# Performance work log

Hardware: AMD Instinct MI355X
Metric: run time of the kernel (lower is better)

Reference implementation:

```python
import jax, jax.numpy as jnp
import numpy as np

NUM_NODES = 100000
EMBED_DIM = 128
HIDDEN = 128
NUM_EDGES = 1600000


def gcn_conv(x, W, b, src, dst, num_nodes):
    """PyG GCNConv: x' = D^{-1/2} (A+I) D^{-1/2} (x W) + b, symmetric norm with self-loops."""
    x = x @ W  # [N, out]
    loops = jnp.arange(num_nodes, dtype=src.dtype)
    s = jnp.concatenate([src, loops])  # sources incl. self-loops
    d = jnp.concatenate([dst, loops])  # targets incl. self-loops
    deg = jax.ops.segment_sum(jnp.ones_like(d, dtype=x.dtype), d, num_segments=num_nodes)
    dis = jnp.where(deg > 0, jax.lax.rsqrt(deg), 0.0)  # deg^{-1/2}, 0 where isolated
    norm = dis[s] * dis[d]  # [E+N]
    msg = x[s] * norm[:, None]  # gather + scale
    out = jax.ops.segment_sum(msg, d, num_segments=num_nodes)  # scatter-add
    return out + b


def setup_inputs() -> dict:
    key = jax.random.key(0)
    k1, k2, k3, k4, k5, k6 = jax.random.split(key, 6)
    edge_index = jax.random.randint(k1, (2, NUM_EDGES), 0, NUM_NODES, dtype=jnp.int64)
    edge_attr = jax.random.normal(k2, (NUM_EDGES,), dtype=jnp.float32)
    emb = jax.random.normal(k3, (NUM_NODES, EMBED_DIM), dtype=jnp.float32) * 0.1
    W1 = jax.random.normal(k4, (EMBED_DIM, HIDDEN), dtype=jnp.float32) * (1.0 / np.sqrt(EMBED_DIM))
    b1 = jnp.zeros((HIDDEN,), dtype=jnp.float32)
    W2 = jax.random.normal(k5, (HIDDEN, HIDDEN), dtype=jnp.float32) * (1.0 / np.sqrt(HIDDEN))
    b2 = jnp.zeros((HIDDEN,), dtype=jnp.float32)
    return {"edge_index": edge_index, "edge_attr": edge_attr, "emb": emb,
            "W1": W1, "b1": b1, "W2": W2, "b2": b2}


def reference(edge_index, edge_attr, emb, W1, b1, W2, b2):
    src, dst = edge_index[0], edge_index[1]
    x = gcn_conv(emb, W1, b1, src, dst, NUM_NODES)
    x = jax.nn.relu(x)
    x = gcn_conv(x, W2, b2, src, dst, NUM_NODES)
    return x
```

## Files before the change

kernel.cpp:

```cpp
#include <hip/hip_runtime.h>

#define EMB 128
#define NBUC 1024
#define NPART 256
#define NSEG 8
#define SEGLEN (NPART / NSEG)
#define PREPB 128

typedef __attribute__((ext_vector_type(8))) short short8;
typedef __attribute__((ext_vector_type(4))) float f32x4;

__device__ __forceinline__ unsigned short f2bf(float f) {
    union { float f; unsigned int i; } v; v.f = f;
    unsigned int x = v.i;
    x += 0x7fffu + ((x >> 16) & 1u);
    return (unsigned short)(x >> 16);
}
__device__ __forceinline__ void acc_fma4(uint2 v, float d,
                                         float& a0, float& a1, float& a2, float& a3) {
    union { unsigned int i; float f; } t;
    t.i = v.x << 16;          a0 = fmaf(d, t.f, a0);
    t.i = v.x & 0xffff0000u;  a1 = fmaf(d, t.f, a1);
    t.i = v.y << 16;          a2 = fmaf(d, t.f, a2);
    t.i = v.y & 0xffff0000u;  a3 = fmaf(d, t.f, a3);
}


__device__ __forceinline__ void p1_body(int bid, int* h, const int* __restrict__ dst,
                                        int* __restrict__ BH, int E, int chunk) {
    for (int i = threadIdx.x; i < NBUC; i += 256) h[i] = 0;
    __syncthreads();
    int s = bid * chunk;
    int e = min(E, s + chunk);
    for (int i = s + threadIdx.x; i < e; i += 256)
        atomicAdd(&h[dst[i] >> 7], 1);
    __syncthreads();
    for (int i = threadIdx.x; i < NBUC; i += 256)
        BH[bid * NBUC + i] = h[i];
}

__device__ __forceinline__ void prepw_body(int bid, const float* __restrict__ W1,
                                           const float* __restrict__ W2,
                                           unsigned short* __restrict__ W1s,
                                           unsigned short* __restrict__ W2s) {
    int gid = bid * 256 + threadIdx.x;
    const float* W = (gid < 16384) ? W1 : W2;
    unsigned short* Ws = (gid < 16384) ? W1s : W2s;
    int idx = gid & 16383;
    int k = idx >> 7, n = idx & 127;
    int kk = k >> 5, q = (k >> 3) & 3, j = k & 7;
    int ct = n >> 4, nn = n & 15;
    int didx = ((((kk * 8 + ct) * 4 + q) * 16 + nn) << 3) + j;
    Ws[didx] = f2bf(W[idx]);
}

__global__ __launch_bounds__(256) void k_start(const int* __restrict__ dst,
                                               int* __restrict__ BH, int E, int chunk,
                                               const float* __restrict__ W1,
                                               const float* __restrict__ W2,
                                               unsigned short* __restrict__ W1s,
                                               unsigned short* __restrict__ W2s) {
    __shared__ int h[NBUC];
    int b = blockIdx.x;
    if (b < NPART) p1_body(b, h, dst, BH, E, chunk);
    else           prepw_body(b - NPART, W1, W2, W1s, W2s);
}

__global__ __launch_bounds__(256) void p_segsum(const int* __restrict__ BH,
                                                int* __restrict__ SS) {
    int idx = blockIdx.x * 256 + threadIdx.x;
    int seg = idx >> 10, b = idx & (NBUC - 1);
    int s = 0;
#pragma unroll 8
    for (int k = 0; k < SEGLEN; ++k)
        s += BH[(seg * SEGLEN + k) * NBUC + b];
    SS[seg * NBUC + b] = s;
}

__global__ __launch_bounds__(1024) void p_scan(const int* __restrict__ SS,
                                               int* __restrict__ base, int E) {
    __shared__ int a[NBUC];
    int t = threadIdx.x;
    int v0 = 0;
#pragma unroll 8
    for (int s = 0; s < NSEG; ++s) v0 += SS[s * NBUC + t];
    a[t] = v0;
    __syncthreads();
    for (int off = 1; off < NBUC; off <<= 1) {
        int v = (t >= off) ? a[t - off] : 0;
        __syncthreads();
        a[t] += v;
        __syncthreads();
    }
    base[t] = a[t] - v0;
    if (t == NBUC - 1) base[NBUC] = E;
}

__global__ __launch_bounds__(256) void p_offs2(int* __restrict__ BH,
                                               const int* __restrict__ SS,
                                               const int* __restrict__ base) {
    int idx = blockIdx.x * 256 + threadIdx.x;
    int seg = idx >> 10, b = idx & (NBUC - 1);
    int run = base[b];
    for (int s = 0; s < seg; ++s) run += SS[s * NBUC + b];
#pragma unroll 4
    for (int k = 0; k < SEGLEN; ++k) {
        int* p = &BH[(seg * SEGLEN + k) * NBUC + b];
        int v = *p;
        *p = run;
        run += v;
    }
}

__device__ __forceinline__ void scatter_body(int bid, int* cnt,
                                             const int* __restrict__ src,
                                             const int* __restrict__ dst,
                                             const int* __restrict__ BH,
                                             int* __restrict__ part,
                                             int E, int chunk) {
    for (int i = threadIdx.x; i < NBUC; i += 256)
        cnt[i] = BH[bid * NBUC + i];
    __syncthreads();
    int s = bid * chunk;
    int e = min(E, s + chunk);
    for (int i = s + threadIdx.x; i < e; i += 256) {
        int d = dst[i];
        int pos = atomicAdd(&cnt[d >> 7], 1);
        part[pos] = src[i] | ((d & 127) << 17);
    }
}

__global__ __launch_bounds__(256) void p3_csr(const int* __restrict__ part,
                                              const int* __restrict__ base,
                                              int* __restrict__ R, int* __restrict__ adj,
                                              float* __restrict__ dis, int N, int E) {
    __shared__ int hist[128];
    __shared__ int sc[128];
    __shared__ int cnt[128];
    int b = blockIdx.x;
    int n0 = b * 128;
    int nn = min(128, N - n0);
    int s = base[b], e = base[b + 1];
    int t = threadIdx.x;

    if (t < 128) hist[t] = 0;
    __syncthreads();
    for (int i = s + t; i < e; i += 256)
        atomicAdd(&hist[part[i] >> 17], 1);
    __syncthreads();

    if (t < 128) sc[t] = hist[t];
    __syncthreads();
    for (int off = 1; off < 128; off <<= 1) {
        int v = 0;
        if (t < 128 && t >= off) v = sc[t - off];
        __syncthreads();
        if (t < 128) sc[t] += v;
        __syncthreads();
    }
    if (t < 128) {
        int excl = sc[t] - hist[t];
        cnt[t] = excl;
        if (t < nn) {
            R[n0 + t] = s + excl;
            dis[n0 + t] = rsqrtf((float)hist[t] + 1.0f);
        }
    }
    if (b == 0 && t == 0) R[N] = E;
    __syncthreads();

    for (int i = s + t; i < e; i += 256) {
        int p = part[i];
        int pos = atomicAdd(&cnt[p >> 17], 1);
        adj[s + pos] = p & 0x1FFFF;
    }
}

template <bool XBF16>
__device__ __forceinline__ void gemm_body(int bid, unsigned short* lds,
    const void* Xv, const unsigned short* __restrict__ Wsw,
    unsigned short* __restrict__ Y, int N)
{
    {
        const uint4* srcp = (const uint4*)Wsw;
        uint4* dstp = (uint4*)lds;
        for (int i = threadIdx.x; i < 2048; i += 256) dstp[i] = srcp[i];
    }
    __syncthreads();

    const int wave = threadIdx.x >> 6;
    const int lane = threadIdx.x & 63;
    const int q = lane >> 4, nn = lane & 15;
    const int row0 = bid * 64 + wave * 16;
    const int arow = row0 + nn;
    const int arc = arow < N ? arow : N - 1;

    f32x4 acc[8];
#pragma unroll
    for (int ct = 0; ct < 8; ++ct) acc[ct] = (f32x4){0.f, 0.f, 0.f, 0.f};

#pragma unroll
    for (int kk = 0; kk < 4; ++kk) {
        short8 af;
        if (XBF16) {
            af = *(const short8*)((const unsigned short*)Xv + (size_t)arc * EMB + kk * 32 + q * 8);
        } else {
            const float* xp = (const float*)Xv + (size_t)arc * EMB + kk * 32 + q * 8;
            float4 u0 = *(const float4*)xp;
            float4 u1 = *(const float4*)(xp + 4);
            af[0] = (short)f2bf(u0.x); af[1] = (short)f2bf(u0.y);
            af[2] = (short)f2bf(u0.z); af[3] = (short)f2bf(u0.w);
            af[4] = (short)f2bf(u1.x); af[5] = (short)f2bf(u1.y);
            af[6] = (short)f2bf(u1.z); af[7] = (short)f2bf(u1.w);
        }
#pragma unroll
        for (int ct = 0; ct < 8; ++ct) {
            short8 bf = ((const short8*)lds)[(kk * 8 + ct) * 64 + lane];
            acc[ct] = __builtin_amdgcn_mfma_f32_16x16x32_bf16(af, bf, acc[ct], 0, 0, 0);
        }
    }

    __syncthreads();

#pragma unroll
    for (int ct = 0; ct < 8; ++ct) {
#pragma unroll
        for (int r = 0; r < 4; ++r) {
            int ml = wave * 16 + q * 4 + r;
            lds[ml * 136 + ct * 16 + nn] = f2bf(acc[ct][r]);
        }
    }
    __syncthreads();

    const int rbase = bid * 64;
    for (int i = threadIdx.x; i < 1024; i += 256) {
        int row = i >> 4, off = i & 15;
        int grow = rbase + row;
        if (grow < N) {
            uint4 v = *(const uint4*)(lds + row * 136 + off * 8);
            *((uint4*)(Y + (size_t)grow * EMB) + off) = v;
        }
    }
}

__global__ __launch_bounds__(256) void k_mid(
    const int* __restrict__ src, const int* __restrict__ dstp,
    const int* __restrict__ BH, int* __restrict__ part, int E, int chunk,
    const void* Xv, const unsigned short* __restrict__ W1s,
    unsigned short* __restrict__ Y, int N)
{
    __shared__ __align__(16) unsigned short smem[16384];
    int b = blockIdx.x;
    if (b < NPART) scatter_body(b, (int*)smem, src, dstp, BH, part, E, chunk);
    else           gemm_body<false>(b - NPART, smem, Xv, W1s, Y, N);
}

__global__ __launch_bounds__(256) void k_gemm2(
    const void* Xv, const unsigned short* __restrict__ Wsw,
    unsigned short* __restrict__ Y, int N)
{
    __shared__ __align__(16) unsigned short smem[16384];
    gemm_body<true>(blockIdx.x, smem, Xv, Wsw, Y, N);
}

template <bool RELU, bool BF16OUT>
__global__ __launch_bounds__(256) void k_gather_finalize(
    const int* __restrict__ R, const int* __restrict__ adj,
    const unsigned short* __restrict__ Y, const float* __restrict__ dis,
    const float* __restrict__ bias, void* __restrict__ Outv, int N)
{
    int t = blockIdx.x * 256 + threadIdx.x;
    int n = t >> 5;
    if (n >= N) return;
    int j = (t & 31) * 4;

    int rs = R[n], re = R[n + 1];
    float dv = dis[n];

    float a0 = 0.f, a1 = 0.f, a2 = 0.f, a3 = 0.f;
    uint2 sv = *(const uint2*)(Y + (size_t)n * EMB + j);
    acc_fma4(sv, dv, a0, a1, a2, a3);

    int e = rs;
    for (; e + 3 < re; e += 4) {
        int s0 = adj[e], s1 = adj[e + 1], s2 = adj[e + 2], s3 = adj[e + 3];
        float d0 = dis[s0], d1 = dis[s1], d2 = dis[s2], d3 = dis[s3];
        uint2 v0 = *(const uint2*)(Y + (size_t)s0 * EMB + j);
        uint2 v1 = *(const uint2*)(Y + (size_t)s1 * EMB + j);
        uint2 v2 = *(const uint2*)(Y + (size_t)s2 * EMB + j);
        uint2 v3 = *(const uint2*)(Y + (size_t)s3 * EMB + j);
        acc_fma4(v0, d0, a0, a1, a2, a3);
        acc_fma4(v1, d1, a0, a1, a2, a3);
        acc_fma4(v2, d2, a0, a1, a2, a3);
        acc_fma4(v3, d3, a0, a1, a2, a3);
    }
    for (; e < re; ++e) {
        int s0 = adj[e];
        float d0 = dis[s0];
        uint2 v0 = *(const uint2*)(Y + (size_t)s0 * EMB + j);
        acc_fma4(v0, d0, a0, a1, a2, a3);
    }

    float4 b = *(const float4*)(bias + j);
    float o0 = dv * a0 + b.x;
    float o1 = dv * a1 + b.y;
    float o2 = dv * a2 + b.z;
    float o3 = dv * a3 + b.w;
    if (RELU) {
        o0 = fmaxf(o0, 0.f); o1 = fmaxf(o1, 0.f);
        o2 = fmaxf(o2, 0.f); o3 = fmaxf(o3, 0.f);
    }
    if (BF16OUT) {
        ushort4 o = { f2bf(o0), f2bf(o1), f2bf(o2), f2bf(o3) };
        *(ushort4*)((unsigned short*)Outv + (size_t)n * EMB + j) = o;
    } else {
        float4 o = { o0, o1, o2, o3 };
        *(float4*)((float*)Outv + (size_t)n * EMB + j) = o;
    }
}

extern "C" void kernel_launch(void* const* d_in, const int* in_sizes, int n_in,
                              void* d_out, int out_size, void* d_ws, size_t ws_size,
                              hipStream_t stream) {
    const int* ei = (const int*)d_in[0];
    const int E = in_sizes[0] / 2;
    const float* emb = (const float*)d_in[2];
    const int N = in_sizes[2] / EMB;
    const float* W1 = (const float*)d_in[3];
    const float* b1 = (const float*)d_in[4];
    const float* W2 = (const float*)d_in[5];
    const float* b2 = (const float*)d_in[6];
    float* out = (float*)d_out;

    const int* src = ei;
    const int* dstp = ei + E;

    char* w = (char*)d_ws;
    auto take = [&](size_t bytes) { char* p = w; w += (bytes + 511) & ~(size_t)511; return p; };
    float* dis  = (float*)take((size_t)N * 4);
    int*   R    = (int*)  take((size_t)(N + 1) * 4);
    int*   base = (int*)  take((size_t)(NBUC + 1) * 4);
    int*   SS   = (int*)  take((size_t)NSEG * NBUC * 4);
    int*   adj  = (int*)  take((size_t)E * 4);
    unsigned short* W1s = (unsigned short*)take((size_t)EMB * EMB * 2);
    unsigned short* W2s = (unsigned short*)take((size_t)EMB * EMB * 2);
    unsigned short* Hb  = (unsigned short*)take((size_t)N * EMB * 2);
    int*   part = (int*)Hb;
    int*   BH   = (int*)((char*)Hb + (((size_t)E * 4 + 511) & ~(size_t)511));
    unsigned short* Y1b = (unsigned short*)d_out;

    const int NB = (N + 127) / 128;
    const int chunk = (E + NPART - 1) / NPART;
    const int gM = (N + 63) / 64;
    const int gG = (N * 32 + 255) / 256;
    const int gS = (NSEG * NBUC) / 256;

    k_start   <<<NPART + PREPB, 256, 0, stream>>>(dstp, BH, E, chunk, W1, W2, W1s, W2s);
    p_segsum  <<<gS, 256, 0, stream>>>(BH, SS);
    p_scan    <<<1, NBUC, 0, stream>>>(SS, base, E);
    p_offs2   <<<gS, 256, 0, stream>>>(BH, SS, base);

    k_mid     <<<NPART + gM, 256, 0, stream>>>(src, dstp, BH, part, E, chunk,
                                               emb, W1s, Y1b, N);
    p3_csr    <<<NB, 256, 0, stream>>>(part, base, R, adj, dis, N, E);

    k_gather_finalize<true, true><<<gG, 256, 0, stream>>>(R, adj, Y1b, dis, b1, Hb, N);

    k_gemm2<<<gM, 256, 0, stream>>>(Hb, W2s, Hb, N);
    k_gather_finalize<false, false><<<gG, 256, 0, stream>>>(R, adj, Hb, dis, b2, out, N);
}
```

Measured before the change: 327.7 us.

## Replace per-partition offset scan with global atomics; fold layer-2 source norm into GEMM

The bucket-offset pipeline changes from per-partition histograms plus segment-sum and offset kernels to a global atomic histogram, a single scan, and per-block atomic reservation of bucket ranges during scatter. This removes two kernel launches and the BH buffer traffic, but the scatter pass now reads dst twice. The layer-2 GEMM now multiplies each output row by dis[row], so the second gather can sum plain bf16 rows without looking up dis per neighbour. The gather loops are also unrolled to 8 neighbours to keep more loads in flight. Edge order inside buckets becomes nondeterministic, but the CSR build re-sorts within each bucket.

```diff
diff --git a/kernel.cpp b/kernel.cpp
--- a/kernel.cpp
+++ b/kernel.cpp
@@ -3,8 +3,6 @@
 #define EMB 128
 #define NBUC 1024
 #define NPART 256
-#define NSEG 8
-#define SEGLEN (NPART / NSEG)
 #define PREPB 128
 
 typedef __attribute__((ext_vector_type(8))) short short8;
@@ -24,10 +22,18 @@
     t.i = v.y << 16;          a2 = fmaf(d, t.f, a2);
     t.i = v.y & 0xffff0000u;  a3 = fmaf(d, t.f, a3);
 }
+__device__ __forceinline__ void acc_bf4(uint2 v,
+                                        float& a0, float& a1, float& a2, float& a3) {
+    union { unsigned int i; float f; } t;
+    t.i = v.x << 16;          a0 += t.f;
+    t.i = v.x & 0xffff0000u;  a1 += t.f;
+    t.i = v.y << 16;          a2 += t.f;
+    t.i = v.y & 0xffff0000u;  a3 += t.f;
+}
 
 
 __device__ __forceinline__ void p1_body(int bid, int* h, const int* __restrict__ dst,
-                                        int* __restrict__ BH, int E, int chunk) {
+                                        int* __restrict__ tot, int E, int chunk) {
     for (int i = threadIdx.x; i < NBUC; i += 256) h[i] = 0;
     __syncthreads();
     int s = bid * chunk;
@@ -35,8 +41,10 @@
     for (int i = s + threadIdx.x; i < e; i += 256)
         atomicAdd(&h[dst[i] >> 7], 1);
     __syncthreads();
-    for (int i = threadIdx.x; i < NBUC; i += 256)
-        BH[bid * NBUC + i] = h[i];
+    for (int i = threadIdx.x; i < NBUC; i += 256) {
+        int v = h[i];
+        if (v) atomicAdd(&tot[i], v);
+    }
 }
 
 __device__ __forceinline__ void prepw_body(int bid, const float* __restrict__ W1,
@@ -55,35 +63,23 @@
 }
 
 __global__ __launch_bounds__(256) void k_start(const int* __restrict__ dst,
-                                               int* __restrict__ BH, int E, int chunk,
+                                               int* __restrict__ tot, int E, int chunk,
                                                const float* __restrict__ W1,
                                                const float* __restrict__ W2,
                                                unsigned short* __restrict__ W1s,
                                                unsigned short* __restrict__ W2s) {
     __shared__ int h[NBUC];
     int b = blockIdx.x;
-    if (b < NPART) p1_body(b, h, dst, BH, E, chunk);
+    if (b < NPART) p1_body(b, h, dst, tot, E, chunk);
     else           prepw_body(b - NPART, W1, W2, W1s, W2s);
 }
 
-__global__ __launch_bounds__(256) void p_segsum(const int* __restrict__ BH,
-                                                int* __restrict__ SS) {
-    int idx = blockIdx.x * 256 + threadIdx.x;
-    int seg = idx >> 10, b = idx & (NBUC - 1);
-    int s = 0;
-#pragma unroll 8
-    for (int k = 0; k < SEGLEN; ++k)
-        s += BH[(seg * SEGLEN + k) * NBUC + b];
-    SS[seg * NBUC + b] = s;
-}
-
-__global__ __launch_bounds__(1024) void p_scan(const int* __restrict__ SS,
-                                               int* __restrict__ base, int E) {
+__global__ __launch_bounds__(1024) void p_scan(const int* __restrict__ tot,
+                                               int* __restrict__ base,
+                                               int* __restrict__ gcnt, int E) {
     __shared__ int a[NBUC];
     int t = threadIdx.x;
-    int v0 = 0;
-#pragma unroll 8
-    for (int s = 0; s < NSEG; ++s) v0 += SS[s * NBUC + t];
+    int v0 = tot[t];
     a[t] = v0;
     __syncthreads();
     for (int off = 1; off < NBUC; off <<= 1) {
@@ -92,37 +88,30 @@
         a[t] += v;
         __syncthreads();
     }
-    base[t] = a[t] - v0;
+    int excl = a[t] - v0;
+    base[t] = excl;
+    gcnt[t] = excl;
     if (t == NBUC - 1) base[NBUC] = E;
-}
-
-__global__ __launch_bounds__(256) void p_offs2(int* __restrict__ BH,
-                                               const int* __restrict__ SS,
-                                               const int* __restrict__ base) {
-    int idx = blockIdx.x * 256 + threadIdx.x;
-    int seg = idx >> 10, b = idx & (NBUC - 1);
-    int run = base[b];
-    for (int s = 0; s < seg; ++s) run += SS[s * NBUC + b];
-#pragma unroll 4
-    for (int k = 0; k < SEGLEN; ++k) {
-        int* p = &BH[(seg * SEGLEN + k) * NBUC + b];
-        int v = *p;
-        *p = run;
-        run += v;
-    }
 }
 
 __device__ __forceinline__ void scatter_body(int bid, int* cnt,
                                              const int* __restrict__ src,
                                              const int* __restrict__ dst,
-                                             const int* __restrict__ BH,
+                                             int* __restrict__ gcnt,
                                              int* __restrict__ part,
                                              int E, int chunk) {
-    for (int i = threadIdx.x; i < NBUC; i += 256)
-        cnt[i] = BH[bid * NBUC + i];
+    for (int i = threadIdx.x; i < NBUC; i += 256) cnt[i] = 0;
     __syncthreads();
     int s = bid * chunk;
     int e = min(E, s + chunk);
+    for (int i = s + threadIdx.x; i < e; i += 256)
+        atomicAdd(&cnt[dst[i] >> 7], 1);
+    __syncthreads();
+    for (int i = threadIdx.x; i < NBUC; i += 256) {
+        int c = cnt[i];
+        cnt[i] = c ? atomicAdd(&gcnt[i], c) : 0;
+    }
+    __syncthreads();
     for (int i = s + threadIdx.x; i < e; i += 256) {
         int d = dst[i];
         int pos = atomicAdd(&cnt[d >> 7], 1);
@@ -176,10 +165,10 @@
     }
 }
 
-template <bool XBF16>
+template <bool XBF16, bool SCALE>
 __device__ __forceinline__ void gemm_body(int bid, unsigned short* lds,
     const void* Xv, const unsigned short* __restrict__ Wsw,
-    unsigned short* __restrict__ Y, int N)
+    const float* __restrict__ dis, unsigned short* __restrict__ Y, int N)
 {
     {
         const uint4* srcp = (const uint4*)Wsw;
@@ -222,12 +211,21 @@
 
     __syncthreads();
 
+    float dv[4];
+    if (SCALE) {
+#pragma unroll
+        for (int r = 0; r < 4; ++r) {
+            int gm = row0 + q * 4 + r;
+            dv[r] = dis[gm < N ? gm : N - 1];
+        }
+    }
 #pragma unroll
     for (int ct = 0; ct < 8; ++ct) {
 #pragma unroll
         for (int r = 0; r < 4; ++r) {
             int ml = wave * 16 + q * 4 + r;
-            lds[ml * 136 + ct * 16 + nn] = f2bf(acc[ct][r]);
+            float val = SCALE ? acc[ct][r] * dv[r] : acc[ct][r];
+            lds[ml * 136 + ct * 16 + nn] = f2bf(val);
         }
     }
     __syncthreads();
@@ -245,25 +243,25 @@
 
 __global__ __launch_bounds__(256) void k_mid(
     const int* __restrict__ src, const int* __restrict__ dstp,
-    const int* __restrict__ BH, int* __restrict__ part, int E, int chunk,
+    int* __restrict__ gcnt, int* __restrict__ part, int E, int chunk,
     const void* Xv, const unsigned short* __restrict__ W1s,
     unsigned short* __restrict__ Y, int N)
 {
     __shared__ __align__(16) unsigned short smem[16384];
     int b = blockIdx.x;
-    if (b < NPART) scatter_body(b, (int*)smem, src, dstp, BH, part, E, chunk);
-    else           gemm_body<false>(b - NPART, smem, Xv, W1s, Y, N);
+    if (b < NPART) scatter_body(b, (int*)smem, src, dstp, gcnt, part, E, chunk);
+    else           gemm_body<false, false>(b - NPART, smem, Xv, W1s, nullptr, Y, N);
 }
 
 __global__ __launch_bounds__(256) void k_gemm2(
     const void* Xv, const unsigned short* __restrict__ Wsw,
-    unsigned short* __restrict__ Y, int N)
+    const float* __restrict__ dis, unsigned short* __restrict__ Y, int N)
 {
     __shared__ __align__(16) unsigned short smem[16384];
-    gemm_body<true>(blockIdx.x, smem, Xv, Wsw, Y, N);
-}
-
-template <bool RELU, bool BF16OUT>
+    gemm_body<true, true>(blockIdx.x, smem, Xv, Wsw, dis, Y, N);
+}
+
+template <bool FOLD, bool RELU, bool BF16OUT>
 __global__ __launch_bounds__(256) void k_gather_finalize(
     const int* __restrict__ R, const int* __restrict__ adj,
     const unsigned short* __restrict__ Y, const float* __restrict__ dis,
@@ -279,26 +277,55 @@
 
     float a0 = 0.f, a1 = 0.f, a2 = 0.f, a3 = 0.f;
     uint2 sv = *(const uint2*)(Y + (size_t)n * EMB + j);
-    acc_fma4(sv, dv, a0, a1, a2, a3);
+    if (FOLD) acc_fma4(sv, dv, a0, a1, a2, a3);
+    else      acc_bf4(sv, a0, a1, a2, a3);
 
     int e = rs;
-    for (; e + 3 < re; e += 4) {
-        int s0 = adj[e], s1 = adj[e + 1], s2 = adj[e + 2], s3 = adj[e + 3];
-        float d0 = dis[s0], d1 = dis[s1], d2 = dis[s2], d3 = dis[s3];
+    for (; e + 7 < re; e += 8) {
+        int s0 = adj[e],     s1 = adj[e + 1], s2 = adj[e + 2], s3 = adj[e + 3];
+        int s4 = adj[e + 4], s5 = adj[e + 5], s6 = adj[e + 6], s7 = adj[e + 7];
         uint2 v0 = *(const uint2*)(Y + (size_t)s0 * EMB + j);
         uint2 v1 = *(const uint2*)(Y + (size_t)s1 * EMB + j);
         uint2 v2 = *(const uint2*)(Y + (size_t)s2 * EMB + j);
         uint2 v3 = *(const uint2*)(Y + (size_t)s3 * EMB + j);
-        acc_fma4(v0, d0, a0, a1, a2, a3);
-        acc_fma4(v1, d1, a0, a1, a2, a3);
-        acc_fma4(v2, d2, a0, a1, a2, a3);
-        acc_fma4(v3, d3, a0, a1, a2, a3);
+        uint2 v4 = *(const uint2*)(Y + (size_t)s4 * EMB + j);
+        uint2 v5 = *(const uint2*)(Y + (size_t)s5 * EMB + j);
+        uint2 v6 = *(const uint2*)(Y + (size_t)s6 * EMB + j);
+        uint2 v7 = *(const uint2*)(Y + (size_t)s7 * EMB + j);
+        if (FOLD) {
+            float d0 = dis[s0], d1 = dis[s1], d2 = dis[s2], d3 = dis[s3];
+            float d4 = dis[s4], d5 = dis[s5], d6 = dis[s6], d7 = dis[s7];
+            acc_fma4(v0, d0, a0, a1, a2, a3); acc_fma4(v1, d1, a0, a1, a2, a3);
+            acc_fma4(v2, d2, a0, a1, a2, a3); acc_fma4(v3, d3, a0, a1, a2, a3);
+            acc_fma4(v4, d4, a0, a1, a2, a3); acc_fma4(v5, d5, a0, a1, a2, a3);
+            acc_fma4(v6, d6, a0, a1, a2, a3); acc_fma4(v7, d7, a0, a1, a2, a3);
+        } else {
+            acc_bf4(v0, a0, a1, a2, a3); acc_bf4(v1, a0, a1, a2, a3);
+            acc_bf4(v2, a0, a1, a2, a3); acc_bf4(v3, a0, a1, a2, a3);
+            acc_bf4(v4, a0, a1, a2, a3); acc_bf4(v5, a0, a1, a2, a3);
+            acc_bf4(v6, a0, a1, a2, a3); acc_bf4(v7, a0, a1, a2, a3);
+        }
+    }
+    for (; e + 3 < re; e += 4) {
+        int s0 = adj[e], s1 = adj[e + 1], s2 = adj[e + 2], s3 = adj[e + 3];
+        uint2 v0 = *(const uint2*)(Y + (size_t)s0 * EMB + j);
+        uint2 v1 = *(const uint2*)(Y + (size_t)s1 * EMB + j);
+        uint2 v2 = *(const uint2*)(Y + (size_t)s2 * EMB + j);
+        uint2 v3 = *(const uint2*)(Y + (size_t)s3 * EMB + j);
+        if (FOLD) {
+            float d0 = dis[s0], d1 = dis[s1], d2 = dis[s2], d3 = dis[s3];
+            acc_fma4(v0, d0, a0, a1, a2, a3); acc_fma4(v1, d1, a0, a1, a2, a3);
+            acc_fma4(v2, d2, a0, a1, a2, a3); acc_fma4(v3, d3, a0, a1, a2, a3);
+        } else {
+            acc_bf4(v0, a0, a1, a2, a3); acc_bf4(v1, a0, a1, a2, a3);
+            acc_bf4(v2, a0, a1, a2, a3); acc_bf4(v3, a0, a1, a2, a3);
+        }
     }
     for (; e < re; ++e) {
         int s0 = adj[e];
-        float d0 = dis[s0];
         uint2 v0 = *(const uint2*)(Y + (size_t)s0 * EMB + j);
-        acc_fma4(v0, d0, a0, a1, a2, a3);
+        if (FOLD) acc_fma4(v0, dis[s0], a0, a1, a2, a3);
+        else      acc_bf4(v0, a0, a1, a2, a3);
     }
 
     float4 b = *(const float4*)(bias + j);
@@ -340,32 +367,33 @@
     float* dis  = (float*)take((size_t)N * 4);
     int*   R    = (int*)  take((size_t)(N + 1) * 4);
     int*   base = (int*)  take((size_t)(NBUC + 1) * 4);
-    int*   SS   = (int*)  take((size_t)NSEG * NBUC * 4);
+    int*   tot  = (int*)  take((size_t)NBUC * 4);
+    int*   gcnt = (int*)  take((size_t)NBUC * 4);
     int*   adj  = (int*)  take((size_t)E * 4);
     unsigned short* W1s = (unsigned short*)take((size_t)EMB * EMB * 2);
     unsigned short* W2s = (unsigned short*)take((size_t)EMB * EMB * 2);
     unsigned short* Hb  = (unsigned short*)take((size_t)N * EMB * 2);
     int*   part = (int*)Hb;
-    int*   BH   = (int*)((char*)Hb + (((size_t)E * 4 + 511) & ~(size_t)511));
     unsigned short* Y1b = (unsigned short*)d_out;
 
     const int NB = (N + 127) / 128;
     const int chunk = (E + NPART - 1) / NPART;
     const int gM = (N + 63) / 64;
     const int gG = (N * 32 + 255) / 256;
-    const int gS = (NSEG * NBUC) / 256;
-
-    k_start   <<<NPART + PREPB, 256, 0, stream>>>(dstp, BH, E, chunk, W1, W2, W1s, W2s);
-    p_segsum  <<<gS, 256, 0, stream>>>(BH, SS);
-    p_scan    <<<1, NBUC, 0, stream>>>(SS, base, E);
-    p_offs2   <<<gS, 256, 0, stream>>>(BH, SS, base);
-
-    k_mid     <<<NPART + gM, 256, 0, stream>>>(src, dstp, BH, part, E, chunk,
-                                               emb, W1s, Y1b, N);
-    p3_csr    <<<NB, 256, 0, stream>>>(part, base, R, adj, dis, N, E);
-
-    k_gather_finalize<true, true><<<gG, 256, 0, stream>>>(R, adj, Y1b, dis, b1, Hb, N);
-
-    k_gemm2<<<gM, 256, 0, stream>>>(Hb, W2s, Hb, N);
-    k_gather_finalize<false, false><<<gG, 256, 0, stream>>>(R, adj, Hb, dis, b2, out, N);
-}
+
+    hipMemsetAsync(tot, 0, (size_t)NBUC * 4, stream);
+
+    k_start<<<NPART + PREPB, 256, 0, stream>>>(dstp, tot, E, chunk, W1, W2, W1s, W2s);
+
+    p_scan<<<1, NBUC, 0, stream>>>(tot, base, gcnt, E);
+
+    k_mid<<<NPART + gM, 256, 0, stream>>>(src, dstp, gcnt, part, E, chunk,
+                                          emb, W1s, Y1b, N);
+
+    p3_csr<<<NB, 256, 0, stream>>>(part, base, R, adj, dis, N, E);
+
+    k_gather_finalize<true, true, true><<<gG, 256, 0, stream>>>(R, adj, Y1b, dis, b1, Hb, N);
+
+    k_gemm2<<<gM, 256, 0, stream>>>(Hb, W2s, dis, Hb, N);
+    k_gather_finalize<false, false, false><<<gG, 256, 0, stream>>>(R, adj, Hb, dis, b2, out, N);
+}
```

After: 327.6 us. Within noise of the previous version (-0.0%).
